# Optimization experiments

Hardware: AMD Instinct MI355X
Metric: run time of the kernel (lower is better)

Reference implementation:

```python
import jax, jax.numpy as jnp
import numpy as np

V, E, H, B, S, SRC, NLEV = 50000, 512, 1024, 64, 32, 256, 5


def setup_inputs() -> dict:
    key = jax.random.key(0)
    ks = jax.random.split(key, 16)
    f = lambda k, sh: jax.random.normal(k, sh, dtype=jnp.float32) * 0.02
    z = lambda n: jnp.zeros((n,), jnp.float32)
    return dict(
        inputs=jax.random.randint(ks[0], (NLEV, B, S), 0, V, dtype=jnp.int32),
        input_lens=jax.random.randint(ks[1], (NLEV, B), 2, S + 1, dtype=jnp.int32),
        contexts=jax.random.normal(ks[2], (B, SRC, H), dtype=jnp.float32),
        emb_W=f(ks[3], (V, E)),
        W_ih0=f(ks[4], (4 * H, E)), W_hh0=f(ks[5], (4 * H, H)), b_ih0=z(4 * H), b_hh0=z(4 * H),
        W_ih1=f(ks[6], (4 * H, H)), W_hh1=f(ks[7], (4 * H, H)), b_ih1=z(4 * H), b_hh1=z(4 * H),
        att_in_W=f(ks[8], (H, H)), att_in_b=z(H),
        att_out_W=f(ks[9], (H, 2 * H)), att_out_b=z(H),
        isl_in_W=f(ks[10], (H, E + H)), isl_in_b=z(H),
        isl_out_W=f(ks[11], (H, H + E)), isl_out_b=z(H),
    )


def _lstm_cell(x, h, c, W_ih, W_hh, b_ih, b_hh):
    # torch.nn.LSTMCell gate order: i, f, g, o
    g = x @ W_ih.T + b_ih + h @ W_hh.T + b_hh
    i, f, gg, o = jnp.split(g, 4, axis=-1)
    c2 = jax.nn.sigmoid(f) * c + jax.nn.sigmoid(i) * jnp.tanh(gg)
    h2 = jax.nn.sigmoid(o) * jnp.tanh(c2)
    return h2, c2


def reference(inputs, input_lens, contexts, emb_W,
              W_ih0, W_hh0, b_ih0, b_hh0, W_ih1, W_hh1, b_ih1, b_hh1,
              att_in_W, att_in_b, att_out_W, att_out_b,
              isl_in_W, isl_in_b, isl_out_W, isl_out_b):
    L, Bb, Ss = inputs.shape
    plevels = inputs[:-1]                       # [L-1, B, S] parent levels
    levels = inputs[1:, :, :-1]                 # [L-1, B, S-1] decoded levels
    plens = input_lens[:-1]                     # [L-1, B]
    # mask[idx][1:l-1] = 1 per original code
    pos = jnp.arange(Ss)
    mask = ((pos[None, None, :] >= 1) & (pos[None, None, :] < (plens[..., None] - 1))).astype(contexts.dtype)
    pembs = emb_W[plevels] * mask[..., None]    # [L-1, B, S, E]
    # init_state: pooled masked parent embeddings + pooled encoder context
    pe = pembs.mean(axis=2)                     # [L-1, B, E]
    cm = jnp.broadcast_to(contexts.mean(axis=1)[None], (L - 1, Bb, contexts.shape[-1]))
    h0 = jnp.tanh(jnp.concatenate([pe, cm], -1) @ isl_in_W.T + isl_in_b)   # [L-1, B, H]
    c0 = jnp.tanh(jnp.concatenate([cm, pe], -1) @ isl_out_W.T + isl_out_b)  # [L-1, B, H]
    h0s = jnp.stack([h0, h0], axis=1)           # [L-1, 2, B, H] same init for both layers
    c0s = jnp.stack([c0, c0], axis=1)

    xs_all = emb_W[levels].transpose(0, 2, 1, 3)  # [L-1, T, B, E]

    def run_level(h0_l, c0_l, xs):
        def step(carry, x):
            h, c = carry                         # [2, B, H] each
            h1, c1 = _lstm_cell(x, h[0], c[0], W_ih0, W_hh0, b_ih0, b_hh0)
            h2, c2 = _lstm_cell(h1, h[1], c[1], W_ih1, W_hh1, b_ih1, b_hh1)
            # global (Luong general) attention
            gamma = h2 @ att_in_W.T + att_in_b   # [B, H]
            w = jax.nn.softmax(jnp.einsum('bsh,bh->bs', contexts, gamma), axis=-1)
            ct = jnp.einsum('bs,bsh->bh', w, contexts)
            out = jnp.tanh(jnp.concatenate([ct, h2], -1) @ att_out_W.T + att_out_b)
            return (jnp.stack([h1, h2]), jnp.stack([c1, c2])), out
        (hT, cT), outs = jax.lax.scan(step, (h0_l, c0_l), xs)
        return outs, hT, cT

    outs, hT, cT = jax.vmap(run_level)(h0s, c0s, xs_all)  # outs: [L-1, T, B, H]
    return outs, hT[-1], cT[-1]
```

## Files before the change

### kernel.cpp

```cpp
#include <hip/hip_runtime.h>
#include <math.h>

#define E 512
#define H 1024
#define B 64
#define S 32
#define SRC 256
#define L4 4
#define T 31
#define R 256

typedef unsigned int uint_t;
typedef unsigned short ushort_t;
typedef float f32x4_v __attribute__((ext_vector_type(4)));
typedef short bf16x8_v __attribute__((ext_vector_type(8)));
typedef _Float16 f16x8_v __attribute__((ext_vector_type(8)));

__device__ __forceinline__ void split1(float x, uint_t& h, uint_t& l) {
    uint_t u = __float_as_uint(x);
    h = u >> 16;
    float hf = __uint_as_float(u & 0xFFFF0000u);
    l = __float_as_uint(x - hf) >> 16;
}

__device__ __forceinline__ void split_quad(float4 v, uint2& hi, uint2& lo) {
    uint_t h0, h1, h2, h3, l0, l1, l2, l3;
    split1(v.x, h0, l0); split1(v.y, h1, l1);
    split1(v.z, h2, l2); split1(v.w, h3, l3);
    hi.x = h0 | (h1 << 16); hi.y = h2 | (h3 << 16);
    lo.x = l0 | (l1 << 16); lo.y = l2 | (l3 << 16);
}

__device__ __forceinline__ ushort_t f16of(float x) {
    _Float16 h = (_Float16)x;
    return *(ushort_t*)&h;
}

__device__ __forceinline__ float2 f16x2f(uint_t u) {
    ushort_t a = (ushort_t)(u & 0xffff), b = (ushort_t)(u >> 16);
    _Float16 fa = *(_Float16*)&a, fb = *(_Float16*)&b;
    return make_float2((float)fa, (float)fb);
}

__device__ __forceinline__ void splitf16(float x, ushort_t& h, ushort_t& l) {
    _Float16 hh = (_Float16)x;
    float hf = (float)hh;
    _Float16 hl = (_Float16)(x - hf);
    h = *(ushort_t*)&hh;
    l = *(ushort_t*)&hl;
}

__device__ __forceinline__ void gl_lds16(const void* g, void* l) {
    __builtin_amdgcn_global_load_lds(
        (const __attribute__((address_space(1))) void*)g,
        (__attribute__((address_space(3))) void*)l, 16, 0, 0);
}

__global__ __launch_bounds__(128) void k_embed(const int* __restrict__ inputs,
                                               const float* __restrict__ embW,
                                               ushort_t* __restrict__ x16) {
    int blk = blockIdx.x;
    int b = blk % B;
    int t = (blk / B) % T;
    int l = blk / (B * T);
    int tok = inputs[(l + 1) * B * S + b * S + t];
    const float4* src = (const float4*)(embW + (long long)tok * E);
    float4 v = src[threadIdx.x];
    uint_t w0 = f16of(v.x) | ((uint_t)f16of(v.y) << 16);
    uint_t w1 = f16of(v.z) | ((uint_t)f16of(v.w) << 16);
    size_t base = ((size_t)t * R + (size_t)l * B + b) * E + threadIdx.x * 4;
    uint2 pk = {w0, w1};
    *(uint2*)(x16 + base) = pk;
}

__global__ __launch_bounds__(128) void k_pe(const int* __restrict__ inputs,
                                            const int* __restrict__ lens,
                                            const float* __restrict__ embW,
                                            ushort_t* __restrict__ phi,
                                            ushort_t* __restrict__ plo) {
    int r = blockIdx.x;
    int l = r >> 6, b = r & 63;
    int plen = lens[l * B + b];
    int send = plen - 1;
    if (send > S) send = S;
    const int* toks = inputs + l * B * S + b * S;
    float4 acc = {0.f, 0.f, 0.f, 0.f};
    for (int s = 1; s < send; ++s) {
        int tok = toks[s];
        float4 v = ((const float4*)(embW + (long long)tok * E))[threadIdx.x];
        acc.x += v.x; acc.y += v.y; acc.z += v.z; acc.w += v.w;
    }
    const float inv = 1.f / 32.f;
    acc.x *= inv; acc.y *= inv; acc.z *= inv; acc.w *= inv;
    uint2 hi, lo; split_quad(acc, hi, lo);
    size_t base = (size_t)r * E + threadIdx.x * 4;
    *(uint2*)(phi + base) = hi;
    *(uint2*)(plo + base) = lo;
}

__global__ __launch_bounds__(256) void k_cm(const float* __restrict__ ctx,
                                            ushort_t* __restrict__ chi,
                                            ushort_t* __restrict__ clo) {
    int b = blockIdx.x;
    int j = threadIdx.x;
    const float4* c4 = (const float4*)(ctx + (size_t)b * SRC * H);
    float4 acc = {0.f, 0.f, 0.f, 0.f};
    for (int s = 0; s < SRC; ++s) {
        float4 v = c4[(size_t)s * (H / 4) + j];
        acc.x += v.x; acc.y += v.y; acc.z += v.z; acc.w += v.w;
    }
    const float inv = 1.f / (float)SRC;
    acc.x *= inv; acc.y *= inv; acc.z *= inv; acc.w *= inv;
    uint2 hi, lo; split_quad(acc, hi, lo);
    size_t base = (size_t)b * H + j * 4;
    *(uint2*)(chi + base) = hi;
    *(uint2*)(clo + base) = lo;
}

__global__ __launch_bounds__(256) void k_wsplit(
    const float* __restrict__ src1, int ld1, int o1, int Ka,
    const float* __restrict__ src2, int ld2, int o2, int Kb,
    int rowmap, ushort_t* __restrict__ dhi, ushort_t* __restrict__ dlo,
    ushort_t* __restrict__ d16) {
    int n = blockIdx.x;
    int KT = Ka + Kb;
    long long r = rowmap ? ((long long)(n & 3) * H + (n >> 2)) : (long long)n;
    for (int k4 = threadIdx.x; k4 < (KT >> 2); k4 += 256) {
        int k = k4 << 2;
        float4 v = (k < Ka) ? *(const float4*)(src1 + r * ld1 + o1 + k)
                            : *(const float4*)(src2 + r * ld2 + o2 + (k - Ka));
        uint2 hi, lo; split_quad(v, hi, lo);
        size_t base = (size_t)n * KT + k;
        *(uint2*)(dhi + base) = hi;
        *(uint2*)(dlo + base) = lo;
        if (d16) {
            uint2 pk;
            pk.x = f16of(v.x) | ((uint_t)f16of(v.y) << 16);
            pk.y = f16of(v.z) | ((uint_t)f16of(v.w) << 16);
            *(uint2*)(d16 + base) = pk;
        }
    }
}

__global__ __launch_bounds__(256) void k_wtile(
    const float* __restrict__ src1, int ld1, int o1, int Ka,
    const float* __restrict__ src2, int ld2, int o2, int Kb,
    int rowmap, unsigned char* __restrict__ panel) {
    int cb = blockIdx.x, t = blockIdx.y;
    int KT = Ka + Kb;
    int NT = KT >> 6;
    size_t obase = ((size_t)cb * NT + t) * 16384;
    int k0 = t << 6;
    for (int q = threadIdx.x; q < 512; q += 256) {
        int s = q >> 6, l = q & 63;
        int n = cb * 64 + 8 * s + (l >> 3);
        long long r = rowmap ? ((long long)(n & 3) * H + (n >> 2)) : (long long)n;
        int xorc = ((l & 7) * 16) ^ ((l >> 3) << 4);
        int ke = k0 + (xorc >> 1);
        const float* sp = (ke < Ka) ? (src1 + r * ld1 + o1 + ke)
                                    : (src2 + r * ld2 + o2 + (ke - Ka));
        float4 v01 = *(const float4*)sp;
        float4 v23 = *(const float4*)(sp + 4);
        uint2 h0, l0, h1, l1;
        split_quad(v01, h0, l0);
        split_quad(v23, h1, l1);
        uint4 hi = {h0.x, h0.y, h1.x, h1.y};
        uint4 lo = {l0.x, l0.y, l1.x, l1.y};
        *(uint4*)(panel + obase + s * 1024 + l * 16) = hi;
        *(uint4*)(panel + obase + 8192 + s * 1024 + l * 16) = lo;
    }
}

__global__ __launch_bounds__(256) void k_wtile16(
    const float* __restrict__ src1, int ld1, int Ka,
    const float* __restrict__ src2, int ld2, int Kb,
    int rowmap, unsigned char* __restrict__ panel) {
    int cb = blockIdx.x, t = blockIdx.y;
    int KT = Ka + Kb;
    int NT = KT >> 6;
    size_t obase = ((size_t)cb * NT + t) * 16384;
    int k0 = t << 6;
    for (int q = threadIdx.x; q < 512; q += 256) {
        int s = q >> 6, l = q & 63;
        int n = cb * 64 + 8 * s + (l >> 3);
        long long r = rowmap ? ((long long)(n & 3) * H + (n >> 2)) : (long long)n;
        int xorc = ((l & 7) * 16) ^ ((l >> 3) << 4);
        int ke = k0 + (xorc >> 1);
        const float* sp = (ke < Ka) ? (src1 + r * ld1 + ke)
                                    : (src2 + r * ld2 + (ke - Ka));
        ushort_t hh[8], ll[8];
#pragma unroll
        for (int e = 0; e < 8; ++e) splitf16(sp[e], hh[e], ll[e]);
        uint4 hi = {(uint_t)hh[0] | ((uint_t)hh[1] << 16),
                    (uint_t)hh[2] | ((uint_t)hh[3] << 16),
                    (uint_t)hh[4] | ((uint_t)hh[5] << 16),
                    (uint_t)hh[6] | ((uint_t)hh[7] << 16)};
        uint4 lo = {(uint_t)ll[0] | ((uint_t)ll[1] << 16),
                    (uint_t)ll[2] | ((uint_t)ll[3] << 16),
                    (uint_t)ll[4] | ((uint_t)ll[5] << 16),
                    (uint_t)ll[6] | ((uint_t)ll[7] << 16)};
        *(uint4*)(panel + obase + s * 1024 + l * 16) = hi;
        *(uint4*)(panel + obase + 8192 + s * 1024 + l * 16) = lo;
    }
}

__global__ __launch_bounds__(256) void k_wtile16s(
    const float* __restrict__ src1, int ld1, int Ka,
    const float* __restrict__ src2, int ld2, int Kb,
    unsigned char* __restrict__ panel) {
    int cb = blockIdx.x, t = blockIdx.y;
    int KT = Ka + Kb;
    int NT = KT >> 6;
    size_t obase = ((size_t)cb * NT + t) * 8192;
    int k0 = t << 6;
    for (int q = threadIdx.x; q < 512; q += 256) {
        int s = q >> 6, l = q & 63;
        int n = cb * 64 + 8 * s + (l >> 3);
        long long r = (long long)(n & 3) * H + (n >> 2);
        int xorc = ((l & 7) * 16) ^ ((l >> 3) << 4);
        int ke = k0 + (xorc >> 1);
        const float* sp = (ke < Ka) ? (src1 + r * ld1 + ke)
                                    : (src2 + r * ld2 + (ke - Ka));
        ushort_t hh[8];
#pragma unroll
        for (int e = 0; e < 8; ++e) hh[e] = f16of(sp[e]);
        uint4 hi = {(uint_t)hh[0] | ((uint_t)hh[1] << 16),
                    (uint_t)hh[2] | ((uint_t)hh[3] << 16),
                    (uint_t)hh[4] | ((uint_t)hh[5] << 16),
                    (uint_t)hh[6] | ((uint_t)hh[7] << 16)};
        *(uint4*)(panel + obase + s * 1024 + l * 16) = hi;
    }
}

__global__ __launch_bounds__(256) void k_g2(
    const ushort_t* __restrict__ Ah1, const ushort_t* __restrict__ Al1, int K1,
    const ushort_t* __restrict__ Ah2, const ushort_t* __restrict__ Al2, int K2,
    int a2mod,
    const unsigned char* __restrict__ Bp,
    const float* __restrict__ bias1, const float* __restrict__ bias2,
    int mode, float* __restrict__ C,
    long long strideT, long long strideL, long long strideB, int act,
    ushort_t* __restrict__ ohi, ushort_t* __restrict__ olo) {
    __shared__ __align__(16) unsigned char lds[65536];
    const int tid = threadIdx.x;
    const int lane = tid & 63;
    const int wv = tid >> 6;
    const int wm = wv & 1, wn = wv >> 1;
    const int cblk = blockIdx.x;
    const int mblk = blockIdx.y;
    const int m0 = mblk * 64;
    const int colbase = cblk * 64;
    const int KT = K1 + K2;
    const int NT = KT >> 6;
    const int n1steps = K1 >> 6;
    const size_t pbase = (size_t)cblk * NT * 16384;

    f32x4_v zero = {0.f, 0.f, 0.f, 0.f};
    f32x4_v acc[2][2] = {{zero, zero}, {zero, zero}};
    const int xorc = ((lane & 7) * 16) ^ ((lane >> 3) << 4);
    const int rsub = lane >> 3;

    auto stage = [&](int t, int buf) {
        unsigned char* dstA = lds + buf * 16384;
        unsigned char* dstB = lds + 32768 + buf * 16384;
        {
            const ushort_t *Ph, *Pl; int lda, k0, mod;
            if (t < n1steps) { Ph = Ah1; Pl = Al1; lda = K1; k0 = t << 6; mod = 0; }
            else { Ph = Ah2; Pl = Al2; lda = K2; k0 = (t - n1steps) << 6; mod = a2mod; }
#pragma unroll
            for (int cc = 0; cc < 4; ++cc) {
                int c = wv * 4 + cc;
                int p = c >> 3, s = c & 7;
                int rr = m0 + 8 * s + rsub;
                if (mod) rr &= (mod - 1);
                const ushort_t* plane = p ? Pl : Ph;
                gl_lds16((const unsigned char*)(plane + (size_t)rr * lda + k0) + xorc,
                         dstA + c * 1024);
            }
        }
        {
            const unsigned char* tb = Bp + pbase + (size_t)t * 16384;
#pragma unroll
            for (int cc = 0; cc < 4; ++cc) {
                int c = wv * 4 + cc;
                gl_lds16(tb + c * 1024 + lane * 16, dstB + c * 1024);
            }
        }
    };
    auto compute = [&](int buf) {
        const unsigned char* Ab = lds + buf * 16384;
        const unsigned char* Bb = lds + 32768 + buf * 16384;
#pragma unroll
        for (int kf = 0; kf < 2; ++kf) {
            int colA = (kf * 64 + ((lane >> 4) * 16)) ^ ((lane & 7) << 4);
            bf16x8_v ah[2], al[2], bh[2], bl[2];
#pragma unroll
            for (int i = 0; i < 2; ++i) {
                int rowm = (wm * 2 + i) * 16 + (lane & 15);
                ah[i] = *(const bf16x8_v*)(Ab + rowm * 128 + colA);
                al[i] = *(const bf16x8_v*)(Ab + 8192 + rowm * 128 + colA);
                int rj = (wn * 2 + i) * 16 + (lane & 15);
                bh[i] = *(const bf16x8_v*)(Bb + rj * 128 + colA);
                bl[i] = *(const bf16x8_v*)(Bb + 8192 + rj * 128 + colA);
            }
            __builtin_amdgcn_s_setprio(1);
#pragma unroll
            for (int i = 0; i < 2; ++i)
#pragma unroll
                for (int j = 0; j < 2; ++j) {
                    acc[i][j] = __builtin_amdgcn_mfma_f32_16x16x32_bf16(al[i], bh[j], acc[i][j], 0, 0, 0);
                    acc[i][j] = __builtin_amdgcn_mfma_f32_16x16x32_bf16(ah[i], bl[j], acc[i][j], 0, 0, 0);
                    acc[i][j] = __builtin_amdgcn_mfma_f32_16x16x32_bf16(ah[i], bh[j], acc[i][j], 0, 0, 0);
                }
            __builtin_amdgcn_s_setprio(0);
        }
    };

    stage(0, 0);
    int cur = 0;
    for (int tt = 0; tt < NT; ++tt) {
        if (tt + 1 < NT) {
            stage(tt + 1, cur ^ 1);
            asm volatile("s_waitcnt vmcnt(8)" ::: "memory");
        } else {
            asm volatile("s_waitcnt vmcnt(0)" ::: "memory");
        }
        __builtin_amdgcn_s_barrier();
        __builtin_amdgcn_sched_barrier(0);
        compute(cur);
        __builtin_amdgcn_sched_barrier(0);
        __builtin_amdgcn_s_barrier();
        cur ^= 1;
    }

    const int l16 = lane & 15, g4 = (lane >> 4) * 4;
#pragma unroll
    for (int i = 0; i < 2; ++i) {
#pragma unroll
        for (int r = 0; r < 4; ++r) {
            int m = m0 + wm * 32 + i * 16 + g4 + r;
            long long rowoff = (long long)(m >> 8) * strideT
                             + (long long)((m >> 6) & 3) * strideL
                             + (long long)(m & 63) * strideB;
#pragma unroll
            for (int jj = 0; jj < 2; ++jj) {
                int n = colbase + wn * 32 + jj * 16 + l16;
                float v = acc[i][jj][r];
                if (mode == 0) {
                    if (bias1) v += bias1[n];
                    if (bias2) v += bias2[n];
                    if (act) v = tanhf(v);
                    C[rowoff + n] = v;
                } else {
                    uint_t hu, lu; split1(v, hu, lu);
                    ohi[rowoff + n] = (ushort_t)hu;
                    olo[rowoff + n] = (ushort_t)lu;
                }
            }
        }
    }
}

__global__ __launch_bounds__(512) void k_g2h(
    const ushort_t* __restrict__ A1, int K1,
    const ushort_t* __restrict__ A2, int K2,
    const unsigned char* __restrict__ Bp,
    const float* __restrict__ bias1,
    int mode, float* __restrict__ C,
    long long strideT, long long strideL, long long strideB,
    ushort_t* __restrict__ ohi, ushort_t* __restrict__ olo) {
    __shared__ __align__(16) unsigned char lds[65536];
    const int tid = threadIdx.x;
    const int lane = tid & 63;
    const int wv = tid >> 6;
    const int wm = wv & 3, wn = wv >> 2;
    const int cblk = blockIdx.x;
    const int m0 = blockIdx.y * 128;
    const int colbase = cblk * 64;
    const int KT = K1 + K2;
    const int NT = KT >> 6;
    const int n1steps = K1 >> 6;
    const size_t pbase = (size_t)cblk * NT * 16384;

    f32x4_v zero = {0.f, 0.f, 0.f, 0.f};
    f32x4_v acc[2][2] = {{zero, zero}, {zero, zero}};
    const int xorc = ((lane & 7) * 16) ^ ((lane >> 3) << 4);
    const int rsub = lane >> 3;

    auto stage = [&](int t, int buf) {
        unsigned char* base = lds + buf * 32768;
        const ushort_t* Ap; int lda, k0;
        if (t < n1steps) { Ap = A1; lda = K1; k0 = t << 6; }
        else             { Ap = A2; lda = K2; k0 = (t - n1steps) << 6; }
        const unsigned char* tb = Bp + pbase + (size_t)t * 16384;
#pragma unroll
        for (int cc = 0; cc < 4; ++cc) {
            int c = wv * 4 + cc;
            if (c < 16) {
                int rr = m0 + 8 * c + rsub;
                gl_lds16((const unsigned char*)(Ap + (size_t)rr * lda + k0) + xorc,
                         base + c * 1024);
            } else {
                int cb = c - 16;
                gl_lds16(tb + cb * 1024 + lane * 16, base + 16384 + cb * 1024);
            }
        }
    };
    auto compute = [&](int buf) {
        const unsigned char* Ab = lds + buf * 32768;
        const unsigned char* Bb = Ab + 16384;
#pragma unroll
        for (int kf = 0; kf < 2; ++kf) {
            int colA = (kf * 64 + ((lane >> 4) * 16)) ^ ((lane & 7) << 4);
            f16x8_v a[2], bh[2], bl[2];
#pragma unroll
            for (int i = 0; i < 2; ++i) {
                int rowm = wm * 32 + i * 16 + (lane & 15);
                a[i] = *(const f16x8_v*)(Ab + rowm * 128 + colA);
                int rj = wn * 32 + i * 16 + (lane & 15);
                bh[i] = *(const f16x8_v*)(Bb + rj * 128 + colA);
                bl[i] = *(const f16x8_v*)(Bb + 8192 + rj * 128 + colA);
            }
            __builtin_amdgcn_s_setprio(1);
#pragma unroll
            for (int i = 0; i < 2; ++i)
#pragma unroll
                for (int j = 0; j < 2; ++j) {
                    acc[i][j] = __builtin_amdgcn_mfma_f32_16x16x32_f16(a[i], bl[j], acc[i][j], 0, 0, 0);
                    acc[i][j] = __builtin_amdgcn_mfma_f32_16x16x32_f16(a[i], bh[j], acc[i][j], 0, 0, 0);
                }
            __builtin_amdgcn_s_setprio(0);
        }
    };

    stage(0, 0);
    int cur = 0;
    for (int tt = 0; tt < NT; ++tt) {
        if (tt + 1 < NT) {
            stage(tt + 1, cur ^ 1);
            asm volatile("s_waitcnt vmcnt(4)" ::: "memory");
        } else {
            asm volatile("s_waitcnt vmcnt(0)" ::: "memory");
        }
        __builtin_amdgcn_s_barrier();
        __builtin_amdgcn_sched_barrier(0);
        compute(cur);
        __builtin_amdgcn_sched_barrier(0);
        __builtin_amdgcn_s_barrier();
        cur ^= 1;
    }

    const int l16 = lane & 15, g4 = (lane >> 4) * 4;
#pragma unroll
    for (int i = 0; i < 2; ++i) {
#pragma unroll
        for (int r = 0; r < 4; ++r) {
            int m = m0 + wm * 32 + i * 16 + g4 + r;
            long long rowoff = (long long)(m >> 8) * strideT
                             + (long long)((m >> 6) & 3) * strideL
                             + (long long)(m & 63) * strideB;
#pragma unroll
            for (int jj = 0; jj < 2; ++jj) {
                int n = colbase + wn * 32 + jj * 16 + l16;
                float v = acc[i][jj][r] + bias1[n];
                if (mode == 0) {
                    C[rowoff + n] = tanhf(v);
                } else {
                    uint_t hu, lu; split1(v, hu, lu);
                    ohi[rowoff + n] = (ushort_t)hu;
                    olo[rowoff + n] = (ushort_t)lu;
                }
            }
        }
    }
}

struct GateJob {
    const ushort_t *A1, *A2;
    const unsigned char* Bp;
    const float *bias1, *bias2;
    float *cbuf, *hf;
    ushort_t *h16;
    int K1, K2;
};

__global__ __launch_bounds__(256) void k_gatepair(GateJob j0, GateJob j1) {
    __shared__ __align__(16) unsigned char lds[65536];
    const bool sec = blockIdx.y >= 4;
    const ushort_t* A1v = sec ? j1.A1 : j0.A1;
    const ushort_t* A2v = sec ? j1.A2 : j0.A2;
    const unsigned char* Bp = sec ? j1.Bp : j0.Bp;
    const float* bias1  = sec ? j1.bias1 : j0.bias1;
    const float* bias2  = sec ? j1.bias2 : j0.bias2;
    float* cbuf         = sec ? j1.cbuf : j0.cbuf;
    float* hf           = sec ? j1.hf   : j0.hf;
    ushort_t* h16       = sec ? j1.h16  : j0.h16;
    const int K1        = sec ? j1.K1   : j0.K1;
    const int K2        = sec ? j1.K2   : j0.K2;

    const int tid = threadIdx.x;
    const int lane = tid & 63;
    const int wv = tid >> 6;
    const int wm = wv & 1, wn = wv >> 1;
    const int mblk = blockIdx.y & 3;
    const int cblk = blockIdx.x;
    const int m0 = mblk * 64;
    const int KT = K1 + K2;
    const int NT = KT >> 6;
    const int n1steps = K1 >> 6;
    const size_t pbase = (size_t)cblk * NT * 8192;

    f32x4_v zero = {0.f, 0.f, 0.f, 0.f};
    f32x4_v acc[2][2] = {{zero, zero}, {zero, zero}};
    const int xorc = ((lane & 7) * 16) ^ ((lane >> 3) << 4);
    const int rsub = lane >> 3;

    auto stage = [&](int t, int buf) {
        unsigned char* base = lds + buf * 16384;
        const ushort_t* Ap; int lda, k0;
        if (t < n1steps) { Ap = A1v; lda = K1; k0 = t << 6; }
        else             { Ap = A2v; lda = K2; k0 = (t - n1steps) << 6; }
        const unsigned char* tb = Bp + pbase + (size_t)t * 8192;
#pragma unroll
        for (int cc = 0; cc < 4; ++cc) {
            int c = wv * 4 + cc;
            if (c < 8) {
                int rr = m0 + 8 * c + rsub;
                gl_lds16((const unsigned char*)(Ap + (size_t)rr * lda + k0) + xorc,
                         base + c * 1024);
            } else {
                gl_lds16(tb + (c - 8) * 1024 + lane * 16, base + c * 1024);
            }
        }
    };
    auto compute = [&](int buf) {
        const unsigned char* Ab = lds + buf * 16384;
        const unsigned char* Bb = Ab + 8192;
#pragma unroll
        for (int kf = 0; kf < 2; ++kf) {
            int colA = (kf * 64 + ((lane >> 4) * 16)) ^ ((lane & 7) << 4);
            f16x8_v a[2], bv[2];
#pragma unroll
            for (int i = 0; i < 2; ++i) {
                int rowm = (wm * 2 + i) * 16 + (lane & 15);
                a[i] = *(const f16x8_v*)(Ab + rowm * 128 + colA);
                int rj = (wn * 2 + i) * 16 + (lane & 15);
                bv[i] = *(const f16x8_v*)(Bb + rj * 128 + colA);
            }
            __builtin_amdgcn_s_setprio(1);
#pragma unroll
            for (int i = 0; i < 2; ++i)
#pragma unroll
                for (int j = 0; j < 2; ++j)
                    acc[i][j] = __builtin_amdgcn_mfma_f32_16x16x32_f16(a[i], bv[j], acc[i][j], 0, 0, 0);
            __builtin_amdgcn_s_setprio(0);
        }
    };

    stage(0, 0);
    stage(1, 1);
    stage(2, 2);
    for (int tt = 0; tt < NT; ++tt) {
        if (tt + 3 < NT) {
            stage(tt + 3, (tt + 3) & 3);
            asm volatile("s_waitcnt vmcnt(12)" ::: "memory");
        } else if (tt + 2 < NT) {
            asm volatile("s_waitcnt vmcnt(8)" ::: "memory");
        } else if (tt + 1 < NT) {
            asm volatile("s_waitcnt vmcnt(4)" ::: "memory");
        } else {
            asm volatile("s_waitcnt vmcnt(0)" ::: "memory");
        }
        __builtin_amdgcn_s_barrier();
        __builtin_amdgcn_sched_barrier(0);
        compute(tt & 3);
        __builtin_amdgcn_sched_barrier(0);
        __builtin_amdgcn_s_barrier();
    }

    float* gtile = (float*)lds;
    const int l16 = lane & 15, g4 = (lane >> 4) * 4;
#pragma unroll
    for (int i = 0; i < 2; ++i)
#pragma unroll
        for (int jj = 0; jj < 2; ++jj)
#pragma unroll
            for (int r = 0; r < 4; ++r)
                gtile[(wm * 32 + i * 16 + g4 + r) * 68 + wn * 32 + jj * 16 + l16] = acc[i][jj][r];
    __syncthreads();

    int m = tid >> 2;
    int hcb = (tid & 3) * 4;
    int nh0 = cblk * 16;
#pragma unroll
    for (int e = 0; e < 4; ++e) {
        int hc = hcb + e;
        float gv[4];
#pragma unroll
        for (int q = 0; q < 4; ++q) {
            int bidx = q * H + nh0 + hc;
            gv[q] = gtile[m * 68 + hc * 4 + q] + bias1[bidx] + bias2[bidx];
        }
        size_t idx = (size_t)(m0 + m) * H + nh0 + hc;
        float cp = cbuf[idx];
        float si = 1.f / (1.f + __expf(-gv[0]));
        float sf = 1.f / (1.f + __expf(-gv[1]));
        float so = 1.f / (1.f + __expf(-gv[3]));
        float c = sf * cp + si * tanhf(gv[2]);
        float hn = so * tanhf(c);
        cbuf[idx] = c;
        hf[idx] = hn;
        h16[idx] = f16of(hn);
    }
}

__global__ __launch_bounds__(256) void k_smfma(
    const ushort_t* __restrict__ gah, const ushort_t* __restrict__ gal,
    const ushort_t* __restrict__ cxh, const ushort_t* __restrict__ cxl,
    float* __restrict__ scores) {
    __shared__ __align__(16) unsigned char lds[65536];
    const int tid = threadIdx.x;
    const int lane = tid & 63;
    const int wv = tid >> 6;
    const int wm = wv & 1, wn = wv >> 1;
    const int b = blockIdx.z;
    const int m0 = blockIdx.y * 64;
    const int colbase = blockIdx.x * 64;
    const int NT = 16;

    f32x4_v zero = {0.f, 0.f, 0.f, 0.f};
    f32x4_v acc[2][2] = {{zero, zero}, {zero, zero}};
    const int xorc = ((lane & 7) * 16) ^ ((lane >> 3) << 4);
    const int rsub = lane >> 3;

    auto stage = [&](int t, int buf) {
        unsigned char* dstA = lds + buf * 16384;
        unsigned char* dstB = lds + 32768 + buf * 16384;
        int k0 = t << 6;
#pragma unroll
        for (int cc = 0; cc < 4; ++cc) {
            int c = wv * 4 + cc;
            int p = c >> 3, s = c & 7;
            int rr = m0 + 8 * s + rsub;
            int tt = rr >> 2; if (tt > 30) tt = 30;
            size_t row = (size_t)tt * R + (rr & 3) * 64 + b;
            const ushort_t* plane = p ? gal : gah;
            gl_lds16((const unsigned char*)(plane + row * H + k0) + xorc,
                     dstA + c * 1024);
        }
#pragma unroll
        for (int cc = 0; cc < 4; ++cc) {
            int c = wv * 4 + cc;
            int p = c >> 3, s = c & 7;
            int rr = colbase + 8 * s + rsub;
            const ushort_t* plane = p ? cxl : cxh;
            gl_lds16((const unsigned char*)(plane + ((size_t)b * SRC + rr) * H + k0) + xorc,
                     dstB + c * 1024);
        }
    };
    auto compute = [&](int buf) {
        const unsigned char* Ab = lds + buf * 16384;
        const unsigned char* Bb = lds + 32768 + buf * 16384;
#pragma unroll
        for (int kf = 0; kf < 2; ++kf) {
            int colA = (kf * 64 + ((lane >> 4) * 16)) ^ ((lane & 7) << 4);
            bf16x8_v ah[2], al[2], bh[2], bl[2];
#pragma unroll
            for (int i = 0; i < 2; ++i) {
                int rowm = (wm * 2 + i) * 16 + (lane & 15);
                ah[i] = *(const bf16x8_v*)(Ab + rowm * 128 + colA);
                al[i] = *(const bf16x8_v*)(Ab + 8192 + rowm * 128 + colA);
                int rj = (wn * 2 + i) * 16 + (lane & 15);
                bh[i] = *(const bf16x8_v*)(Bb + rj * 128 + colA);
                bl[i] = *(const bf16x8_v*)(Bb + 8192 + rj * 128 + colA);
            }
            __builtin_amdgcn_s_setprio(1);
#pragma unroll
            for (int i = 0; i < 2; ++i)
#pragma unroll
                for (int j = 0; j < 2; ++j) {
                    acc[i][j] = __builtin_amdgcn_mfma_f32_16x16x32_bf16(al[i], bh[j], acc[i][j], 0, 0, 0);
                    acc[i][j] = __builtin_amdgcn_mfma_f32_16x16x32_bf16(ah[i], bl[j], acc[i][j], 0, 0, 0);
                    acc[i][j] = __builtin_amdgcn_mfma_f32_16x16x32_bf16(ah[i], bh[j], acc[i][j], 0, 0, 0);
                }
            __builtin_amdgcn_s_setprio(0);
        }
    };

    stage(0, 0);
    int cur = 0;
    for (int tt = 0; tt < NT; ++tt) {
        if (tt + 1 < NT) {
            stage(tt + 1, cur ^ 1);
            asm volatile("s_waitcnt vmcnt(8)" ::: "memory");
        } else {
            asm volatile("s_waitcnt vmcnt(0)" ::: "memory");
        }
        __builtin_amdgcn_s_barrier();
        __builtin_amdgcn_sched_barrier(0);
        compute(cur);
        __builtin_amdgcn_sched_barrier(0);
        __builtin_amdgcn_s_barrier();
        cur ^= 1;
    }

    const int l16 = lane & 15, g4 = (lane >> 4) * 4;
#pragma unroll
    for (int i = 0; i < 2; ++i) {
#pragma unroll
        for (int jj = 0; jj < 2; ++jj) {
#pragma unroll
            for (int r = 0; r < 4; ++r) {
                int m = m0 + wm * 32 + i * 16 + g4 + r;
                int t = m >> 2;
                if (t < 31) {
                    size_t row = (size_t)t * R + (m & 3) * 64 + b;
                    int n = colbase + wn * 32 + jj * 16 + l16;
                    scores[row * SRC + n] = acc[i][jj][r];
                }
            }
        }
    }
}

__global__ __launch_bounds__(256) void k_smax(const float* __restrict__ scores,
                                              float* __restrict__ w) {
    int t = blockIdx.x, b = blockIdx.y;
    int l = threadIdx.x >> 6, lane = threadIdx.x & 63;
    size_t row = (size_t)t * R + l * 64 + b;
    const float* sr = scores + row * SRC;
    float v0 = sr[lane];
    float v1 = sr[lane + 64];
    float v2 = sr[lane + 128];
    float v3 = sr[lane + 192];
    float m = fmaxf(fmaxf(v0, v1), fmaxf(v2, v3));
#pragma unroll
    for (int off = 32; off >= 1; off >>= 1) m = fmaxf(m, __shfl_xor(m, off));
    float e0 = expf(v0 - m), e1 = expf(v1 - m), e2 = expf(v2 - m), e3 = expf(v3 - m);
    float sum = e0 + e1 + e2 + e3;
#pragma unroll
    for (int off = 32; off >= 1; off >>= 1) sum += __shfl_xor(sum, off);
    float inv = 1.f / sum;
    float* wr = w + row * SRC;
    wr[lane] = e0 * inv;
    wr[lane + 64] = e1 * inv;
    wr[lane + 128] = e2 * inv;
    wr[lane + 192] = e3 * inv;
}

__global__ __launch_bounds__(512) void k_ct_all(const ushort_t* __restrict__ ctx16,
                                                const float* __restrict__ w,
                                                ushort_t* __restrict__ ct16) {
    __shared__ float ws[32][260];
    const int b = blockIdx.x, tc = blockIdx.y;
    const int tid = threadIdx.x;
    for (int q = tid; q < 32 * 64; q += 512) {
        int r = q >> 6, c4 = q & 63;
        int t = tc * 8 + (r >> 2);
        float4 v = {0.f, 0.f, 0.f, 0.f};
        if (t < 31)
            v = *(const float4*)(w + ((size_t)t * R + (r & 3) * 64 + b) * SRC + c4 * 4);
        *(float4*)&ws[r][c4 * 4] = v;
    }
    __syncthreads();

    float2 acc[32];
#pragma unroll
    for (int r = 0; r < 32; ++r) acc[r] = make_float2(0.f, 0.f);
    const uint_t* base = (const uint_t*)(ctx16 + (size_t)b * SRC * H) + tid;
    for (int s = 0; s < SRC; s += 4) {
        float2 c0 = f16x2f(base[(size_t)s * (H / 2)]);
        float2 c1 = f16x2f(base[(size_t)(s + 1) * (H / 2)]);
        float2 c2 = f16x2f(base[(size_t)(s + 2) * (H / 2)]);
        float2 c3 = f16x2f(base[(size_t)(s + 3) * (H / 2)]);
#pragma unroll
        for (int r = 0; r < 32; ++r) {
            float4 wv = *(const float4*)&ws[r][s];
            acc[r].x += wv.x * c0.x + wv.y * c1.x + wv.z * c2.x + wv.w * c3.x;
            acc[r].y += wv.x * c0.y + wv.y * c1.y + wv.z * c2.y + wv.w * c3.y;
        }
    }
#pragma unroll
    for (int r = 0; r < 32; ++r) {
        int t = tc * 8 + (r >> 2);
        if (t < 31) {
            size_t obase = ((size_t)t * R + (r & 3) * 64 + b) * H + tid * 2;
            uint_t pk = f16of(acc[r].x) | ((uint_t)f16of(acc[r].y) << 16);
            *(uint_t*)(ct16 + obase) = pk;
        }
    }
}

__global__ __launch_bounds__(256) void k_init_split(const float* __restrict__ h0f,
                                                    const float* __restrict__ c0f,
                                                    float* __restrict__ h1f,
                                                    float* __restrict__ c1f,
                                                    ushort_t* __restrict__ h0_16,
                                                    ushort_t* __restrict__ h1i_16) {
    int idx = blockIdx.x * 256 + threadIdx.x;
    float h = h0f[idx], c = c0f[idx];
    h1f[idx] = h; c1f[idx] = c;
    ushort_t hv = f16of(h);
    h0_16[idx] = hv;
    h1i_16[idx] = hv;
}

extern "C" void kernel_launch(void* const* d_in, const int* in_sizes, int n_in,
                              void* d_out, int out_size, void* d_ws, size_t ws_size,
                              hipStream_t stream) {
    const int*   inputs     = (const int*)d_in[0];
    const int*   input_lens = (const int*)d_in[1];
    const float* contexts   = (const float*)d_in[2];
    const float* emb_W      = (const float*)d_in[3];
    const float* W_ih0      = (const float*)d_in[4];
    const float* W_hh0      = (const float*)d_in[5];
    const float* b_ih0      = (const float*)d_in[6];
    const float* b_hh0      = (const float*)d_in[7];
    const float* W_ih1      = (const float*)d_in[8];
    const float* W_hh1      = (const float*)d_in[9];
    const float* b_ih1      = (const float*)d_in[10];
    const float* b_hh1      = (const float*)d_in[11];
    const float* att_in_W   = (const float*)d_in[12];
    const float* att_in_b   = (const float*)d_in[13];
    const float* att_out_W  = (const float*)d_in[14];
    const float* att_out_b  = (const float*)d_in[15];
    const float* isl_in_W   = (const float*)d_in[16];
    const float* isl_in_b   = (const float*)d_in[17];
    const float* isl_out_W  = (const float*)d_in[18];
    const float* isl_out_b  = (const float*)d_in[19];

    float* out = (float*)d_out;

    char* p = (char*)d_ws;
    auto alloc = [&](size_t bytes) { char* r = p; p += (bytes + 255) & ~(size_t)255; return r; };
    ushort_t* xs16 = (ushort_t*)alloc((size_t)T * R * E * 2);
    ushort_t* h016[2];
    h016[0] = (ushort_t*)alloc((size_t)R * H * 2);
    h016[1] = (ushort_t*)alloc((size_t)R * H * 2);
    ushort_t* h1i16 = (ushort_t*)alloc((size_t)R * H * 2);
    ushort_t* h116all = (ushort_t*)alloc((size_t)T * R * H * 2);
    ushort_t* gamh = (ushort_t*)alloc((size_t)T * R * H * 2);
    ushort_t* gaml = (ushort_t*)alloc((size_t)T * R * H * 2);
    ushort_t* pehi = (ushort_t*)alloc((size_t)R * E * 2);
    ushort_t* pelo = (ushort_t*)alloc((size_t)R * E * 2);
    ushort_t* cmhi = (ushort_t*)alloc((size_t)B * H * 2);
    ushort_t* cmlo = (ushort_t*)alloc((size_t)B * H * 2);
    unsigned char* wg0p = (unsigned char*)alloc((size_t)64 * 24 * 8192);
    unsigned char* wg1p = (unsigned char*)alloc((size_t)64 * 32 * 8192);
    unsigned char* wgip = (unsigned char*)alloc((size_t)16 * 16 * 16384);
    unsigned char* wotp = (unsigned char*)alloc((size_t)16 * 32 * 16384);
    unsigned char* wiip = (unsigned char*)alloc((size_t)16 * 24 * 16384);
    unsigned char* wiop = (unsigned char*)alloc((size_t)16 * 24 * 16384);
    ushort_t* cxh = (ushort_t*)alloc((size_t)B * SRC * H * 2);
    ushort_t* cxl = (ushort_t*)alloc((size_t)B * SRC * H * 2);
    ushort_t* ctx16 = (ushort_t*)alloc((size_t)B * SRC * H * 2);
    float* h0f = (float*)alloc((size_t)R * H * 4);
    float* h1f = (float*)alloc((size_t)R * H * 4);
    float* c0f = (float*)alloc((size_t)R * H * 4);
    float* c1f = (float*)alloc((size_t)R * H * 4);
    float* scores = (float*)alloc((size_t)T * R * SRC * 4);
    float* wbuf   = (float*)alloc((size_t)T * R * SRC * 4);
    ushort_t* ct16 = (ushort_t*)alloc((size_t)T * R * H * 2);

    k_embed<<<L4 * T * B, 128, 0, stream>>>(inputs, emb_W, xs16);
    k_pe<<<R, 128, 0, stream>>>(inputs, input_lens, emb_W, pehi, pelo);
    k_cm<<<B, 256, 0, stream>>>(contexts, cmhi, cmlo);
    k_wtile16s<<<dim3(64, 24), 256, 0, stream>>>(W_ih0, 512, 512, W_hh0, 1024, 1024, wg0p);
    k_wtile16s<<<dim3(64, 32), 256, 0, stream>>>(W_ih1, 1024, 1024, W_hh1, 1024, 1024, wg1p);
    k_wtile16<<<dim3(16, 16), 256, 0, stream>>>(att_in_W, 1024, 1024, nullptr, 0, 0, 0, wgip);
    k_wtile16<<<dim3(16, 32), 256, 0, stream>>>(att_out_W, 2048, 2048, nullptr, 0, 0, 0, wotp);
    k_wtile<<<dim3(16, 24), 256, 0, stream>>>(isl_in_W, 1536, 0, 1536, nullptr, 0, 0, 0, 0, wiip);
    k_wtile<<<dim3(16, 24), 256, 0, stream>>>(isl_out_W, 1536, 1024, 512, isl_out_W, 1536, 0, 1024, 0, wiop);
    k_wsplit<<<B * SRC, 256, 0, stream>>>(contexts, 1024, 0, 1024, nullptr, 0, 0, 0, 0, cxh, cxl, ctx16);

    k_g2<<<dim3(16, 4), 256, 0, stream>>>(pehi, pelo, 512, cmhi, cmlo, 1024, 64,
                                          wiip, isl_in_b, nullptr, 0,
                                          h0f, 0, 64LL * H, (long long)H, 1,
                                          nullptr, nullptr);
    k_g2<<<dim3(16, 4), 256, 0, stream>>>(pehi, pelo, 512, cmhi, cmlo, 1024, 64,
                                          wiop, isl_out_b, nullptr, 0,
                                          c0f, 0, 64LL * H, (long long)H, 1,
                                          nullptr, nullptr);
    k_init_split<<<R * H / 256, 256, 0, stream>>>(h0f, c0f, h1f, c1f, h016[0], h1i16);

    int cur = 0;
    for (int L = 0; L <= T; ++L) {
        bool has0 = (L < T), has1 = (L > 0);
        GateJob g0 = {}, g1 = {};
        if (has0) {
            g0.A1 = xs16 + (size_t)L * R * E;
            g0.A2 = h016[cur];
            g0.Bp = wg0p;
            g0.bias1 = b_ih0;  g0.bias2 = b_hh0;
            g0.cbuf = c0f;  g0.hf = h0f;
            g0.h16 = h016[cur ^ 1];
            g0.K1 = E;  g0.K2 = H;
        }
        if (has1) {
            g1.A1 = h016[cur];
            g1.A2 = (L == 1) ? h1i16 : h116all + (size_t)(L - 2) * R * H;
            g1.Bp = wg1p;
            g1.bias1 = b_ih1;  g1.bias2 = b_hh1;
            g1.cbuf = c1f;  g1.hf = h1f;
            g1.h16 = h116all + (size_t)(L - 1) * R * H;
            g1.K1 = H;  g1.K2 = H;
        }
        if (has0 && has1)
            k_gatepair<<<dim3(64, 8), 256, 0, stream>>>(g0, g1);
        else if (has0)
            k_gatepair<<<dim3(64, 4), 256, 0, stream>>>(g0, g0);
        else
            k_gatepair<<<dim3(64, 4), 256, 0, stream>>>(g1, g1);
        if (has0) cur ^= 1;
    }

    k_g2h<<<dim3(16, 62), 512, 0, stream>>>(h116all, 1024, h116all, 0,
                                            wgip, att_in_b, 2,
                                            nullptr, 256LL * H, 64LL * H, (long long)H,
                                            gamh, gaml);
    k_smfma<<<dim3(4, 2, B), 256, 0, stream>>>(gamh, gaml, cxh, cxl, scores);
    k_smax<<<dim3(T, B), 256, 0, stream>>>(scores, wbuf);
    k_ct_all<<<dim3(B, 4), 512, 0, stream>>>(ctx16, wbuf, ct16);
    k_g2h<<<dim3(16, 62), 512, 0, stream>>>(ct16, 1024, h116all, 1024,
                                            wotp, att_out_b, 0,
                                            out, (long long)B * H,
                                            (long long)T * B * H, (long long)H,
                                            nullptr, nullptr);

    size_t OUTS = (size_t)L4 * T * B * H;
    size_t seg = (size_t)B * H;
    hipMemcpyAsync(out + OUTS,           h0f + 192 * H, seg * 4, hipMemcpyDeviceToDevice, stream);
    hipMemcpyAsync(out + OUTS + seg,     h1f + 192 * H, seg * 4, hipMemcpyDeviceToDevice, stream);
    hipMemcpyAsync(out + OUTS + 2 * seg, c0f + 192 * H, seg * 4, hipMemcpyDeviceToDevice, stream);
    hipMemcpyAsync(out + OUTS + 3 * seg, c1f + 192 * H, seg * 4, hipMemcpyDeviceToDevice, stream);
}
```

Before: 1.173 ms.

## Compute attention context with f16 MFMA GEMM over transposed contexts

```diff
diff --git a/kernel.cpp b/kernel.cpp
--- a/kernel.cpp
+++ b/kernel.cpp
@@ -34,12 +34,6 @@
 __device__ __forceinline__ ushort_t f16of(float x) {
     _Float16 h = (_Float16)x;
     return *(ushort_t*)&h;
-}
-
-__device__ __forceinline__ float2 f16x2f(uint_t u) {
-    ushort_t a = (ushort_t)(u & 0xffff), b = (ushort_t)(u >> 16);
-    _Float16 fa = *(_Float16*)&a, fb = *(_Float16*)&b;
-    return make_float2((float)fa, (float)fb);
 }
 
 __device__ __forceinline__ void splitf16(float x, ushort_t& h, ushort_t& l) {
@@ -139,6 +133,26 @@
             pk.y = f16of(v.z) | ((uint_t)f16of(v.w) << 16);
             *(uint2*)(d16 + base) = pk;
         }
+    }
+}
+
+__global__ __launch_bounds__(256) void k_ctxT(const ushort_t* __restrict__ src,
+                                              ushort_t* __restrict__ dst) {
+    __shared__ ushort_t tile[64][66];
+    const int b = blockIdx.x, h0 = blockIdx.y * 64, s0 = blockIdx.z * 64;
+    const int tid = threadIdx.x;
+    for (int it = tid; it < 512; it += 256) {
+        int s = it >> 3, ho = (it & 7) * 8;
+        uint4 v = *(const uint4*)(src + ((size_t)b * SRC + s0 + s) * H + h0 + ho);
+        *(uint4*)&tile[s][ho] = v;
+    }
+    __syncthreads();
+    for (int it = tid; it < 512; it += 256) {
+        int h = it >> 3, so = (it & 7) * 8;
+        ushort_t vals[8];
+#pragma unroll
+        for (int i = 0; i < 8; ++i) vals[i] = tile[so + i][h];
+        *(uint4*)(dst + ((size_t)b * H + h0 + h) * SRC + s0 + so) = *(uint4*)vals;
     }
 }
 
@@ -724,7 +738,7 @@
 }
 
 __global__ __launch_bounds__(256) void k_smax(const float* __restrict__ scores,
-                                              float* __restrict__ w) {
+                                              ushort_t* __restrict__ w16) {
     int t = blockIdx.x, b = blockIdx.y;
     int l = threadIdx.x >> 6, lane = threadIdx.x & 63;
     size_t row = (size_t)t * R + l * 64 + b;
@@ -741,52 +755,106 @@
 #pragma unroll
     for (int off = 32; off >= 1; off >>= 1) sum += __shfl_xor(sum, off);
     float inv = 1.f / sum;
-    float* wr = w + row * SRC;
-    wr[lane] = e0 * inv;
-    wr[lane + 64] = e1 * inv;
-    wr[lane + 128] = e2 * inv;
-    wr[lane + 192] = e3 * inv;
-}
-
-__global__ __launch_bounds__(512) void k_ct_all(const ushort_t* __restrict__ ctx16,
-                                                const float* __restrict__ w,
-                                                ushort_t* __restrict__ ct16) {
-    __shared__ float ws[32][260];
-    const int b = blockIdx.x, tc = blockIdx.y;
+    ushort_t* wr = w16 + row * SRC;
+    wr[lane] = f16of(e0 * inv);
+    wr[lane + 64] = f16of(e1 * inv);
+    wr[lane + 128] = f16of(e2 * inv);
+    wr[lane + 192] = f16of(e3 * inv);
+}
+
+__global__ __launch_bounds__(256) void k_ctmm(
+    const ushort_t* __restrict__ w16, const ushort_t* __restrict__ ctxT,
+    ushort_t* __restrict__ ct16) {
+    __shared__ __align__(16) unsigned char lds[32768];
     const int tid = threadIdx.x;
-    for (int q = tid; q < 32 * 64; q += 512) {
-        int r = q >> 6, c4 = q & 63;
-        int t = tc * 8 + (r >> 2);
-        float4 v = {0.f, 0.f, 0.f, 0.f};
-        if (t < 31)
-            v = *(const float4*)(w + ((size_t)t * R + (r & 3) * 64 + b) * SRC + c4 * 4);
-        *(float4*)&ws[r][c4 * 4] = v;
-    }
-    __syncthreads();
-
-    float2 acc[32];
-#pragma unroll
-    for (int r = 0; r < 32; ++r) acc[r] = make_float2(0.f, 0.f);
-    const uint_t* base = (const uint_t*)(ctx16 + (size_t)b * SRC * H) + tid;
-    for (int s = 0; s < SRC; s += 4) {
-        float2 c0 = f16x2f(base[(size_t)s * (H / 2)]);
-        float2 c1 = f16x2f(base[(size_t)(s + 1) * (H / 2)]);
-        float2 c2 = f16x2f(base[(size_t)(s + 2) * (H / 2)]);
-        float2 c3 = f16x2f(base[(size_t)(s + 3) * (H / 2)]);
-#pragma unroll
-        for (int r = 0; r < 32; ++r) {
-            float4 wv = *(const float4*)&ws[r][s];
-            acc[r].x += wv.x * c0.x + wv.y * c1.x + wv.z * c2.x + wv.w * c3.x;
-            acc[r].y += wv.x * c0.y + wv.y * c1.y + wv.z * c2.y + wv.w * c3.y;
-        }
-    }
-#pragma unroll
-    for (int r = 0; r < 32; ++r) {
-        int t = tc * 8 + (r >> 2);
-        if (t < 31) {
-            size_t obase = ((size_t)t * R + (r & 3) * 64 + b) * H + tid * 2;
-            uint_t pk = f16of(acc[r].x) | ((uint_t)f16of(acc[r].y) << 16);
-            *(uint_t*)(ct16 + obase) = pk;
+    const int lane = tid & 63;
+    const int wv = tid >> 6;
+    const int wm = wv & 1, wn = wv >> 1;
+    const int b = blockIdx.z;
+    const int m0 = blockIdx.y * 64;
+    const int colbase = blockIdx.x * 64;
+    const int NT = 4;
+
+    f32x4_v zero = {0.f, 0.f, 0.f, 0.f};
+    f32x4_v acc[2][2] = {{zero, zero}, {zero, zero}};
+    const int xorc = ((lane & 7) * 16) ^ ((lane >> 3) << 4);
+    const int rsub = lane >> 3;
+
+    auto stage = [&](int t, int buf) {
+        unsigned char* base = lds + buf * 16384;
+        int k0 = t << 6;
+#pragma unroll
+        for (int cc = 0; cc < 4; ++cc) {
+            int c = wv * 4 + cc;
+            if (c < 8) {
+                int rr = m0 + 8 * c + rsub;
+                int tt = rr >> 2; if (tt > 30) tt = 30;
+                size_t row = (size_t)tt * R + (rr & 3) * 64 + b;
+                gl_lds16((const unsigned char*)(w16 + row * SRC + k0) + xorc,
+                         base + c * 1024);
+            } else {
+                int hr = colbase + 8 * (c - 8) + rsub;
+                gl_lds16((const unsigned char*)(ctxT + ((size_t)b * H + hr) * SRC + k0) + xorc,
+                         base + 8192 + (c - 8) * 1024);
+            }
+        }
+    };
+    auto compute = [&](int buf) {
+        const unsigned char* Ab = lds + buf * 16384;
+        const unsigned char* Bb = Ab + 8192;
+#pragma unroll
+        for (int kf = 0; kf < 2; ++kf) {
+            int colA = (kf * 64 + ((lane >> 4) * 16)) ^ ((lane & 7) << 4);
+            f16x8_v a[2], bv[2];
+#pragma unroll
+            for (int i = 0; i < 2; ++i) {
+                int rowm = (wm * 2 + i) * 16 + (lane & 15);
+                a[i] = *(const f16x8_v*)(Ab + rowm * 128 + colA);
+                int rj = (wn * 2 + i) * 16 + (lane & 15);
+                bv[i] = *(const f16x8_v*)(Bb + rj * 128 + colA);
+            }
+            __builtin_amdgcn_s_setprio(1);
+#pragma unroll
+            for (int i = 0; i < 2; ++i)
+#pragma unroll
+                for (int j = 0; j < 2; ++j)
+                    acc[i][j] = __builtin_amdgcn_mfma_f32_16x16x32_f16(a[i], bv[j], acc[i][j], 0, 0, 0);
+            __builtin_amdgcn_s_setprio(0);
+        }
+    };
+
+    stage(0, 0);
+    int cur = 0;
+    for (int tt = 0; tt < NT; ++tt) {
+        if (tt + 1 < NT) {
+            stage(tt + 1, cur ^ 1);
+            asm volatile("s_waitcnt vmcnt(4)" ::: "memory");
+        } else {
+            asm volatile("s_waitcnt vmcnt(0)" ::: "memory");
+        }
+        __builtin_amdgcn_s_barrier();
+        __builtin_amdgcn_sched_barrier(0);
+        compute(cur);
+        __builtin_amdgcn_sched_barrier(0);
+        __builtin_amdgcn_s_barrier();
+        cur ^= 1;
+    }
+
+    const int l16 = lane & 15, g4 = (lane >> 4) * 4;
+#pragma unroll
+    for (int i = 0; i < 2; ++i) {
+#pragma unroll
+        for (int r = 0; r < 4; ++r) {
+            int m = m0 + wm * 32 + i * 16 + g4 + r;
+            int t = m >> 2;
+            if (t < 31) {
+                size_t row = (size_t)t * R + (m & 3) * 64 + b;
+#pragma unroll
+                for (int jj = 0; jj < 2; ++jj) {
+                    int n = colbase + wn * 32 + jj * 16 + l16;
+                    ct16[row * H + n] = f16of(acc[i][jj][r]);
+                }
+            }
         }
     }
 }
@@ -854,12 +922,13 @@
     ushort_t* cxh = (ushort_t*)alloc((size_t)B * SRC * H * 2);
     ushort_t* cxl = (ushort_t*)alloc((size_t)B * SRC * H * 2);
     ushort_t* ctx16 = (ushort_t*)alloc((size_t)B * SRC * H * 2);
+    ushort_t* ctxT16 = (ushort_t*)alloc((size_t)B * SRC * H * 2);
     float* h0f = (float*)alloc((size_t)R * H * 4);
     float* h1f = (float*)alloc((size_t)R * H * 4);
     float* c0f = (float*)alloc((size_t)R * H * 4);
     float* c1f = (float*)alloc((size_t)R * H * 4);
     float* scores = (float*)alloc((size_t)T * R * SRC * 4);
-    float* wbuf   = (float*)alloc((size_t)T * R * SRC * 4);
+    ushort_t* w16 = (ushort_t*)alloc((size_t)T * R * SRC * 2);
     ushort_t* ct16 = (ushort_t*)alloc((size_t)T * R * H * 2);
 
     k_embed<<<L4 * T * B, 128, 0, stream>>>(inputs, emb_W, xs16);
@@ -872,6 +941,7 @@
     k_wtile<<<dim3(16, 24), 256, 0, stream>>>(isl_in_W, 1536, 0, 1536, nullptr, 0, 0, 0, 0, wiip);
     k_wtile<<<dim3(16, 24), 256, 0, stream>>>(isl_out_W, 1536, 1024, 512, isl_out_W, 1536, 0, 1024, 0, wiop);
     k_wsplit<<<B * SRC, 256, 0, stream>>>(contexts, 1024, 0, 1024, nullptr, 0, 0, 0, 0, cxh, cxl, ctx16);
+    k_ctxT<<<dim3(B, 16, 4), 256, 0, stream>>>(ctx16, ctxT16);
 
     k_g2<<<dim3(16, 4), 256, 0, stream>>>(pehi, pelo, 512, cmhi, cmlo, 1024, 64,
                                           wiip, isl_in_b, nullptr, 0,
@@ -919,8 +989,8 @@
                                             nullptr, 256LL * H, 64LL * H, (long long)H,
                                             gamh, gaml);
     k_smfma<<<dim3(4, 2, B), 256, 0, stream>>>(gamh, gaml, cxh, cxl, scores);
-    k_smax<<<dim3(T, B), 256, 0, stream>>>(scores, wbuf);
-    k_ct_all<<<dim3(B, 4), 512, 0, stream>>>(ctx16, wbuf, ct16);
+    k_smax<<<dim3(T, B), 256, 0, stream>>>(scores, w16);
+    k_ctmm<<<dim3(16, 2, B), 256, 0, stream>>>(w16, ctxT16, ct16);
     k_g2h<<<dim3(16, 62), 512, 0, stream>>>(ct16, 1024, h116all, 1024,
                                             wotp, att_out_b, 0,
                                             out, (long long)B * H,
```

After: 1.136 ms. 3.2% less time.
